# Kernel tuning notes

Hardware: AMD Instinct MI355X
Metric: run time of the kernel (lower is better)

The kernel has to match this reference:

```python
import jax, jax.numpy as jnp
import numpy as np

EPS = 1e-8  # matches F.cosine_similarity default eps
SIM_TARGET = 1  # int(self.sim_matrix), a scalar constant


def setup_inputs() -> dict:
    key = jax.random.key(0)
    k1, k2 = jax.random.split(key)
    input1 = jax.random.normal(k1, (4096, 1024), dtype=jnp.float32)  # [U, P]
    input2 = jax.random.normal(k2, (4096, 1024), dtype=jnp.float32)  # [V, P]
    return {"input1": input1, "input2": input2}


def reference(input1, input2):
    # Row-normalize with eps clamp (same as F.cosine_similarity per pair)
    n1 = input1 / jnp.maximum(jnp.linalg.norm(input1, axis=1, keepdims=True), EPS)
    n2 = input2 / jnp.maximum(jnp.linalg.norm(input2, axis=1, keepdims=True), EPS)
    cos = jnp.einsum('up,vp->uv', n1, n2)  # [U, V] pairwise cosine similarity
    return jnp.sum((SIM_TARGET - cos) ** 2)
```

## Files before the change

### kernel.cpp

```cpp
#include <hip/hip_runtime.h>
#include <hip/hip_bf16.h>
#include <stdint.h>

#define U_ROWS 4096
#define P_DIM  1024
#define TB     256
#define BK     64
#define NKT    (P_DIM / BK)

typedef int i32x4  __attribute__((ext_vector_type(4)));
typedef int i32x16 __attribute__((ext_vector_type(16)));

__global__ __launch_bounds__(256) void norm_i8_kernel(
    const float* __restrict__ in1, const float* __restrict__ in2,
    int8_t* __restrict__ out, float* __restrict__ loss_out) {
    const int w = threadIdx.x >> 6, lane = threadIdx.x & 63;
    const int row = blockIdx.x * 4 + w;
    const float* src = (row < U_ROWS) ? (in1 + (size_t)row * P_DIM)
                                      : (in2 + (size_t)(row - U_ROWS) * P_DIM);
    float4 v[4];
    float ss = 0.0f;
    #pragma unroll
    for (int j = 0; j < 4; ++j) {
        v[j] = ((const float4*)src)[lane * 4 + j];
        ss += v[j].x * v[j].x + v[j].y * v[j].y + v[j].z * v[j].z + v[j].w * v[j].w;
    }
    #pragma unroll
    for (int off = 32; off > 0; off >>= 1) ss += __shfl_xor(ss, off, 64);
    const float inv = 512.0f / fmaxf(sqrtf(ss), 1e-8f);

    i32x4 d;
    #pragma unroll
    for (int j = 0; j < 4; ++j) {
        int q0 = max(-127, min(127, (int)rintf(v[j].x * inv)));
        int q1 = max(-127, min(127, (int)rintf(v[j].y * inv)));
        int q2 = max(-127, min(127, (int)rintf(v[j].z * inv)));
        int q3 = max(-127, min(127, (int)rintf(v[j].w * inv)));
        d[j] = (q0 & 255) | ((q1 & 255) << 8) | ((q2 & 255) << 16) | (q3 << 24);
    }
    const int w0   = lane >> 2;
    const int g    = lane & 3;
    const int slot = g ^ ((row >> 1) & 3);
    *(i32x4*)(out + (size_t)row * P_DIM + w0 * 64 + slot * 16) = d;
    if (blockIdx.x == 0 && threadIdx.x == 0) *loss_out = 0.0f;
}

__global__ __launch_bounds__(512) void cosloss_gemm_i8(
    const int8_t* __restrict__ n1, const int8_t* __restrict__ n2,
    float* __restrict__ loss_out) {
    __shared__ __align__(16) uint8_t As[3][TB * BK];
    __shared__ __align__(16) uint8_t Bs[3][TB * BK];

    const int tid  = threadIdx.x;
    const int w    = tid >> 6;
    const int lane = tid & 63;

    const int id  = blockIdx.x;
    const int xcd = id & 7;
    const int t   = id >> 3;
    const int cb  = xcd * 2 + (t & 1);
    const int rb  = t >> 1;

    const uint8_t* gA = (const uint8_t*)n1 + (size_t)rb * TB * P_DIM;
    const uint8_t* gB = (const uint8_t*)n2 + (size_t)cb * TB * P_DIM;

    const int srow = lane >> 2;
    const int scol = (lane & 3) * 16;
    const int c0   = w * 4;

    auto stage = [&](int kt, int b) {
        #pragma unroll
        for (int cc = 0; cc < 4; ++cc) {
            const int c = c0 + cc;
            const uint8_t* gsrc = (c < 16)
                ? gA + (size_t)(c * 16 + srow) * P_DIM + kt * BK + scol
                : gB + (size_t)((c - 16) * 16 + srow) * P_DIM + kt * BK + scol;
            uint8_t* sdst = (c < 16) ? As[b] + c * 1024 : Bs[b] + (c - 16) * 1024;
            __builtin_amdgcn_global_load_lds(
                (const __attribute__((address_space(1))) void*)gsrc,
                (__attribute__((address_space(3))) void*)sdst, 16, 0, 0);
        }
    };

    i32x16 acc[4][2];
    #pragma unroll
    for (int mi = 0; mi < 4; ++mi)
        #pragma unroll
        for (int ni = 0; ni < 2; ++ni)
            acc[mi][ni] = (i32x16){0,0,0,0,0,0,0,0,0,0,0,0,0,0,0,0};

    const int wr = (w & 1) * 128;
    const int wc = (w >> 1) * 64;
    const int lm = lane & 31;
    const int lh = lane >> 5;

    int aoff[4][2], boff[2][2];
    #pragma unroll
    for (int i = 0; i < 4; ++i) {
        const int m = wr + i * 32 + lm;
        #pragma unroll
        for (int s = 0; s < 2; ++s)
            aoff[i][s] = m * BK + (((2 * s + lh) ^ ((m >> 1) & 3)) * 16);
    }
    #pragma unroll
    for (int ni = 0; ni < 2; ++ni) {
        const int n = wc + ni * 32 + lm;
        #pragma unroll
        for (int s = 0; s < 2; ++s)
            boff[ni][s] = n * BK + (((2 * s + lh) ^ ((n >> 1) & 3)) * 16);
    }

    stage(0, 0);
    stage(1, 1);

    #pragma unroll
    for (int kt = 0; kt < NKT; ++kt) {
        if (kt < NKT - 1) {
            asm volatile("s_waitcnt vmcnt(4)" ::: "memory");
        } else {
            asm volatile("s_waitcnt vmcnt(0)" ::: "memory");
        }
        __builtin_amdgcn_s_barrier();
        __builtin_amdgcn_sched_barrier(0);

        const uint8_t* Ab = As[kt % 3];
        const uint8_t* Bb = Bs[kt % 3];

        i32x4 af[2][4], bf[2][2];
        #pragma unroll
        for (int i = 0; i < 4; ++i)
            af[0][i] = *(const i32x4*)(Ab + aoff[i][0]);
        #pragma unroll
        for (int ni = 0; ni < 2; ++ni)
            bf[0][ni] = *(const i32x4*)(Bb + boff[ni][0]);
        if (kt + 2 < NKT) stage(kt + 2, (kt + 2) % 3);
        #pragma unroll
        for (int i = 0; i < 4; ++i)
            af[1][i] = *(const i32x4*)(Ab + aoff[i][1]);
        #pragma unroll
        for (int ni = 0; ni < 2; ++ni)
            bf[1][ni] = *(const i32x4*)(Bb + boff[ni][1]);

        __builtin_amdgcn_sched_barrier(0);
        __builtin_amdgcn_s_setprio(1);
        #pragma unroll
        for (int mi = 0; mi < 4; ++mi)
            #pragma unroll
            for (int ni = 0; ni < 2; ++ni)
                acc[mi][ni] = __builtin_amdgcn_mfma_i32_32x32x32_i8(
                    af[0][mi], bf[0][ni], acc[mi][ni], 0, 0, 0);
        __builtin_amdgcn_s_setprio(0);

        __builtin_amdgcn_sched_barrier(0);
        __builtin_amdgcn_s_setprio(1);
        #pragma unroll
        for (int mi = 0; mi < 4; ++mi)
            #pragma unroll
            for (int ni = 0; ni < 2; ++ni)
                acc[mi][ni] = __builtin_amdgcn_mfma_i32_32x32x32_i8(
                    af[1][mi], bf[1][ni], acc[mi][ni], 0, 0, 0);
        __builtin_amdgcn_s_setprio(0);
    }

    float local = 0.0f;
    #pragma unroll
    for (int mi = 0; mi < 4; ++mi)
        #pragma unroll
        for (int ni = 0; ni < 2; ++ni)
            #pragma unroll
            for (int r = 0; r < 16; ++r) {
                const float dd = 1.0f - (float)acc[mi][ni][r] * (1.0f / 262144.0f);
                local += dd * dd;
            }
    #pragma unroll
    for (int off = 32; off > 0; off >>= 1) local += __shfl_down(local, off, 64);

    __syncthreads();
    float* redf = (float*)As;
    if (lane == 0) redf[w] = local;
    __syncthreads();
    if (tid == 0) {
        float tsum = 0.0f;
        #pragma unroll
        for (int i = 0; i < 8; ++i) tsum += redf[i];
        atomicAdd(loss_out, tsum);
    }
}

extern "C" void kernel_launch(void* const* d_in, const int* in_sizes, int n_in,
                              void* d_out, int out_size, void* d_ws, size_t ws_size,
                              hipStream_t stream) {
    const float* in1 = (const float*)d_in[0];
    const float* in2 = (const float*)d_in[1];
    float* out = (float*)d_out;
    int8_t* nrm = (int8_t*)d_ws;

    norm_i8_kernel<<<(U_ROWS * 2) / 4, 256, 0, stream>>>(in1, in2, nrm, out);

    cosloss_gemm_i8<<<(U_ROWS / TB) * (U_ROWS / TB), 512, 0, stream>>>(
        nrm, nrm + (size_t)U_ROWS * P_DIM, out);
}
```

Baseline: 94.94 us.

## Software-pipeline LDS fragment loads across k-tiles to overlap with MFMA

Restructures the int8 GEMM main loop so the first half-K fragments of the next tile are read from LDS between the two MFMA groups of the current tile. The vmcnt wait and barrier move to mid-iteration, so LDS read latency overlaps MFMA execution instead of stalling at the start of each tile. This adds register pressure from the persistent fragment arrays. It also changes barrier placement, which could interact with the triple-buffer reuse timing.

After: 93.20 us. About the same (-1.8%).

```diff
diff --git a/kernel.cpp b/kernel.cpp
--- a/kernel.cpp
+++ b/kernel.cpp
@@ -110,37 +110,31 @@
             boff[ni][s] = n * BK + (((2 * s + lh) ^ ((n >> 1) & 3)) * 16);
     }
 
+    i32x4 fra[2][4], frb[2][2];
+
     stage(0, 0);
     stage(1, 1);
+    asm volatile("s_waitcnt vmcnt(4)" ::: "memory");
+    __builtin_amdgcn_s_barrier();
+    __builtin_amdgcn_sched_barrier(0);
+    #pragma unroll
+    for (int i = 0; i < 4; ++i) fra[0][i] = *(const i32x4*)(As[0] + aoff[i][0]);
+    #pragma unroll
+    for (int ni = 0; ni < 2; ++ni) frb[0][ni] = *(const i32x4*)(Bs[0] + boff[ni][0]);
 
     #pragma unroll
     for (int kt = 0; kt < NKT; ++kt) {
-        if (kt < NKT - 1) {
-            asm volatile("s_waitcnt vmcnt(4)" ::: "memory");
-        } else {
-            asm volatile("s_waitcnt vmcnt(0)" ::: "memory");
-        }
-        __builtin_amdgcn_s_barrier();
-        __builtin_amdgcn_sched_barrier(0);
-
+        const int pc = (2 * kt) & 1;
         const uint8_t* Ab = As[kt % 3];
         const uint8_t* Bb = Bs[kt % 3];
 
-        i32x4 af[2][4], bf[2][2];
-        #pragma unroll
-        for (int i = 0; i < 4; ++i)
-            af[0][i] = *(const i32x4*)(Ab + aoff[i][0]);
-        #pragma unroll
-        for (int ni = 0; ni < 2; ++ni)
-            bf[0][ni] = *(const i32x4*)(Bb + boff[ni][0]);
+        if (kt > 0) __builtin_amdgcn_s_barrier();
+        __builtin_amdgcn_sched_barrier(0);
+        #pragma unroll
+        for (int i = 0; i < 4; ++i) fra[1][i] = *(const i32x4*)(Ab + aoff[i][1]);
+        #pragma unroll
+        for (int ni = 0; ni < 2; ++ni) frb[1][ni] = *(const i32x4*)(Bb + boff[ni][1]);
         if (kt + 2 < NKT) stage(kt + 2, (kt + 2) % 3);
-        #pragma unroll
-        for (int i = 0; i < 4; ++i)
-            af[1][i] = *(const i32x4*)(Ab + aoff[i][1]);
-        #pragma unroll
-        for (int ni = 0; ni < 2; ++ni)
-            bf[1][ni] = *(const i32x4*)(Bb + boff[ni][1]);
-
         __builtin_amdgcn_sched_barrier(0);
         __builtin_amdgcn_s_setprio(1);
         #pragma unroll
@@ -148,18 +142,36 @@
             #pragma unroll
             for (int ni = 0; ni < 2; ++ni)
                 acc[mi][ni] = __builtin_amdgcn_mfma_i32_32x32x32_i8(
-                    af[0][mi], bf[0][ni], acc[mi][ni], 0, 0, 0);
+                    fra[0][mi], frb[0][ni], acc[mi][ni], 0, 0, 0);
         __builtin_amdgcn_s_setprio(0);
-
-        __builtin_amdgcn_sched_barrier(0);
+        __builtin_amdgcn_sched_barrier(0);
+
+        if (kt < NKT - 1) {
+            if (kt + 2 < NKT) {
+                asm volatile("s_waitcnt vmcnt(4)" ::: "memory");
+            } else {
+                asm volatile("s_waitcnt vmcnt(0)" ::: "memory");
+            }
+            __builtin_amdgcn_s_barrier();
+            __builtin_amdgcn_sched_barrier(0);
+            const uint8_t* An = As[(kt + 1) % 3];
+            const uint8_t* Bn = Bs[(kt + 1) % 3];
+            #pragma unroll
+            for (int i = 0; i < 4; ++i) fra[0][i] = *(const i32x4*)(An + aoff[i][0]);
+            #pragma unroll
+            for (int ni = 0; ni < 2; ++ni) frb[0][ni] = *(const i32x4*)(Bn + boff[ni][0]);
+            __builtin_amdgcn_sched_barrier(0);
+        }
         __builtin_amdgcn_s_setprio(1);
         #pragma unroll
         for (int mi = 0; mi < 4; ++mi)
             #pragma unroll
             for (int ni = 0; ni < 2; ++ni)
                 acc[mi][ni] = __builtin_amdgcn_mfma_i32_32x32x32_i8(
-                    af[1][mi], bf[1][ni], acc[mi][ni], 0, 0, 0);
+                    fra[1][mi], frb[1][ni], acc[mi][ni], 0, 0, 0);
         __builtin_amdgcn_s_setprio(0);
+        __builtin_amdgcn_sched_barrier(0);
+        (void)pc;
     }
 
     float local = 0.0f;
```
